# Kernel optimization log

Hardware: AMD Instinct MI355X
Metric: run time of the kernel (lower is better)

The kernel has to match this reference:

```python
import jax, jax.numpy as jnp
import numpy as np

B = 8192   # particle ensemble (vmapped y0)
T = 64     # timesteps
D = 2      # data_size
W = 128    # width_size
CAP = 5.0  # cap() clamps trajectories to a bounded domain


def setup_inputs() -> dict:
    key = jax.random.key(0)
    ks = jax.random.split(key, 10)
    s_in = 1.0 / np.sqrt(D)
    s_h = 1.0 / np.sqrt(W)
    u = jax.random.uniform
    return {
        "ts": jnp.linspace(0.0, 1.0, T, dtype=jnp.float32),
        "y0": jax.random.normal(ks[0], (B, D), jnp.float32),
        "W1": u(ks[1], (W, D), jnp.float32, -s_in, s_in),
        "b1": u(ks[2], (W,), jnp.float32, -s_in, s_in),
        "W2": u(ks[3], (W, W), jnp.float32, -s_h, s_h),
        "b2": u(ks[4], (W,), jnp.float32, -s_h, s_h),
        "W3": u(ks[5], (W, W), jnp.float32, -s_h, s_h),
        "b3": u(ks[6], (W,), jnp.float32, -s_h, s_h),
        "W4": u(ks[7], (D, W), jnp.float32, -s_h, s_h),
        "b4": u(ks[8], (D,), jnp.float32, -s_h, s_h),
    }


def _func(y, W1, b1, W2, b2, W3, b3, W4, b4):
    # eqx.nn.MLP(data_size -> data_size, width_size, depth=3),
    # activation=leaky_relu, final_activation=identity. y: [B, D]
    h = jax.nn.leaky_relu(y @ W1.T + b1)
    h = jax.nn.leaky_relu(h @ W2.T + b2)
    h = jax.nn.leaky_relu(h @ W3.T + b3)
    return h @ W4.T + b4


def reference(ts, y0, W1, b1, W2, b2, W3, b3, W4, b4):
    # MultiTerm(drift, ODETerm(func)) with Euler on the uniform grid ts:
    #   y_{n+1} = y_n + dt_n * (drift(t_n, y_n) + func(t_n, y_n))
    # drift vector field: f(t, y) = -y
    dts = ts[1:] - ts[:-1]  # [T-1]

    def step(y, dt):
        dy = -y + _func(y, W1, b1, W2, b2, W3, b3, W4, b4)
        y_new = y + dt * dy
        return y_new, y_new

    _, ys_tail = jax.lax.scan(step, y0, dts)          # [T-1, B, D]
    ys = jnp.concatenate([y0[None], ys_tail], axis=0)  # [T, B, D] == solution.ys
    return jnp.clip(ys, -CAP, CAP)  # cap(solution.ys)
```

## Files before the change

kernel.cpp:

```cpp
#include <hip/hip_runtime.h>

#define NB 8192
#define NT 64
#define FCAP 5.0f

typedef unsigned int u32;
typedef float f32x4 __attribute__((ext_vector_type(4)));
typedef __bf16 bf16x8 __attribute__((ext_vector_type(8)));
typedef u32 u32x4 __attribute__((ext_vector_type(4)));
typedef u32 u32x2 __attribute__((ext_vector_type(2)));

static __device__ __forceinline__ u32 pk2(float lo, float hi) {
  u32 r;
  asm("v_cvt_pk_bf16_f32 %0, %1, %2" : "=v"(r) : "v"(lo), "v"(hi));
  return r;
}
static __device__ __forceinline__ float clipc(float a) { return fminf(fmaxf(a, -FCAP), FCAP); }

static __device__ __forceinline__ bf16x8 mkfrag(const float* __restrict__ p) {
  f32x4 a = *(const f32x4*)p, b = *(const f32x4*)(p + 4);
  u32x4 wv = {pk2(a[0], a[1]), pk2(a[2], a[3]), pk2(b[0], b[1]), pk2(b[2], b[3])};
  return __builtin_bit_cast(bf16x8, wv);
}

#define MFMA16(A, B, C) __builtin_amdgcn_mfma_f32_16x16x32_bf16(A, B, C, 0, 0, 0)

#define LRELU4(C)                                                  \
  _Pragma("unroll") for (int r_ = 0; r_ < 4; ++r_) {               \
    C[r_] = fmaxf(C[r_], 0.01f * C[r_]);                           \
  }

__global__ __launch_bounds__(256, 2) void ode_kernel(
    const float* __restrict__ ts, const float* __restrict__ y0,
    const float* __restrict__ W1, const float* __restrict__ b1,
    const float* __restrict__ W2, const float* __restrict__ b2,
    const float* __restrict__ W3, const float* __restrict__ b3,
    const float* __restrict__ W4, const float* __restrict__ b4,
    float* __restrict__ out) {
  const int tid = threadIdx.x;
  const int wv = __builtin_amdgcn_readfirstlane(tid >> 6);
  const int l = tid & 63;
  const int g = l >> 4;
  const int c = l & 15;
  const int gp0 = blockIdx.x * 16;

  __shared__ alignas(16) u32 bufA[16 * 68];
  __shared__ alignas(16) u32 bufB[16 * 68];
  __shared__ alignas(16) float fbuf[16 * 8];

  bf16x8 aW2[2][4], aW3[2][4];
#pragma unroll
  for (int mt = 0; mt < 2; ++mt) {
    const int R = 32 * wv + 16 * mt + c;
#pragma unroll
    for (int kt = 0; kt < 4; ++kt) {
      aW2[mt][kt] = mkfrag(W2 + R * 128 + 32 * kt + 8 * g);
      aW3[mt][kt] = mkfrag(W3 + R * 128 + 32 * kt + 8 * g);
    }
  }
  bf16x8 aW1[2];
#pragma unroll
  for (int mt = 0; mt < 2; ++mt) {
    const int R = 32 * wv + 16 * mt + c;
    u32x4 f = {0, 0, 0, 0};
    if (g == 0) {
      f[0] = pk2(W1[2 * R], W1[2 * R + 1]);
      f[1] = pk2(b1[R], 0.f);
    }
    aW1[mt] = __builtin_bit_cast(bf16x8, f);
  }
  bf16x8 aW4;
  {
    u32x4 f = {0, 0, 0, 0};
    if (c < 2) {
      const float* s = W4 + c * 128 + 32 * wv + 8 * g;
      f32x4 a = *(const f32x4*)s, b = *(const f32x4*)(s + 4);
      f = (u32x4){pk2(a[0], a[1]), pk2(a[2], a[3]), pk2(b[0], b[1]), pk2(b[2], b[3])};
    }
    aW4 = __builtin_bit_cast(bf16x8, f);
  }
  f32x4 cb2[2], cb3[2];
#pragma unroll
  for (int mt = 0; mt < 2; ++mt) {
#pragma unroll
    for (int r = 0; r < 4; ++r) {
      const int row = 32 * wv + 16 * mt + 4 * g + r;
      cb2[mt][r] = b2[row];
      cb3[mt][r] = b3[row];
    }
  }
  const float b40 = b4[0], b41 = b4[1];

  float y1 = y0[(gp0 + c) * 2];
  float y2 = y0[(gp0 + c) * 2 + 1];

  if (wv == 0 && g == 0) {
    float2 st = {clipc(y1), clipc(y2)};
    *(float2*)(out + (gp0 + c) * 2) = st;
  }

  const f32x4 zero4 = {0.f, 0.f, 0.f, 0.f};
  const int wbase = 68 * c + 16 * wv + 2 * g;
  const int rbase = 68 * c + 4 * g;

#pragma unroll 1
  for (int t = 0; t < NT - 1; ++t) {
    const float dt = ts[t + 1] - ts[t];

    u32x4 byw = {0, 0, 0, 0};
    if (g == 0) {
      byw[0] = pk2(y1, y2);
      byw[1] = 0x3f80u;
    }
    const bf16x8 By = __builtin_bit_cast(bf16x8, byw);
    f32x4 C0 = MFMA16(aW1[0], By, zero4);
    f32x4 C1 = MFMA16(aW1[1], By, zero4);
    LRELU4(C0);
    LRELU4(C1);
    *(__shared__ u32x2*)&bufA[wbase]     = (u32x2){pk2(C0[0], C0[1]), pk2(C0[2], C0[3])};
    *(__shared__ u32x2*)&bufA[wbase + 8] = (u32x2){pk2(C1[0], C1[1]), pk2(C1[2], C1[3])};
    __syncthreads();

    f32x4 D0 = cb2[0], D1 = cb2[1];
#pragma unroll
    for (int kt = 0; kt < 4; ++kt) {
      const bf16x8 q =
          __builtin_bit_cast(bf16x8, *(const __shared__ u32x4*)&bufA[rbase + 16 * kt]);
      D0 = MFMA16(aW2[0][kt], q, D0);
      D1 = MFMA16(aW2[1][kt], q, D1);
    }
    LRELU4(D0);
    LRELU4(D1);
    *(__shared__ u32x2*)&bufB[wbase]     = (u32x2){pk2(D0[0], D0[1]), pk2(D0[2], D0[3])};
    *(__shared__ u32x2*)&bufB[wbase + 8] = (u32x2){pk2(D1[0], D1[1]), pk2(D1[2], D1[3])};
    __syncthreads();

    f32x4 E0 = cb3[0], E1 = cb3[1];
#pragma unroll
    for (int kt = 0; kt < 4; ++kt) {
      const bf16x8 q =
          __builtin_bit_cast(bf16x8, *(const __shared__ u32x4*)&bufB[rbase + 16 * kt]);
      E0 = MFMA16(aW3[0][kt], q, E0);
      E1 = MFMA16(aW3[1][kt], q, E1);
    }
    LRELU4(E0);
    LRELU4(E1);
    *(__shared__ u32x2*)&bufA[wbase]     = (u32x2){pk2(E0[0], E0[1]), pk2(E0[2], E0[3])};
    *(__shared__ u32x2*)&bufA[wbase + 8] = (u32x2){pk2(E1[0], E1[1]), pk2(E1[2], E1[3])};

    const bf16x8 q3 =
        __builtin_bit_cast(bf16x8, *(const __shared__ u32x4*)&bufA[rbase + 16 * wv]);
    f32x4 C4 = MFMA16(aW4, q3, zero4);
    if (g == 0)
      *(__shared__ float2*)&fbuf[c * 8 + wv * 2] = (float2){C4[0], C4[1]};
    __syncthreads();

    const float4 pa = *(const __shared__ float4*)&fbuf[c * 8];
    const float4 pb = *(const __shared__ float4*)&fbuf[c * 8 + 4];
    const float f0 = b40 + pa.x + pa.z + pb.x + pb.z;
    const float f1v = b41 + pa.y + pa.w + pb.y + pb.w;
    y1 += dt * (f0 - y1);
    y2 += dt * (f1v - y2);

    if (wv == 0 && g == 0) {
      float2 st = {clipc(y1), clipc(y2)};
      *(float2*)(out + (t + 1) * (NB * 2) + (gp0 + c) * 2) = st;
    }
  }
}

extern "C" void kernel_launch(void* const* d_in, const int* in_sizes, int n_in,
                              void* d_out, int out_size, void* d_ws, size_t ws_size,
                              hipStream_t stream) {
  const float* ts = (const float*)d_in[0];
  const float* y0 = (const float*)d_in[1];
  const float* W1 = (const float*)d_in[2];
  const float* b1 = (const float*)d_in[3];
  const float* W2 = (const float*)d_in[4];
  const float* b2 = (const float*)d_in[5];
  const float* W3 = (const float*)d_in[6];
  const float* b3 = (const float*)d_in[7];
  const float* W4 = (const float*)d_in[8];
  const float* b4 = (const float*)d_in[9];

  ode_kernel<<<NB / 16, 256, 0, stream>>>(ts, y0, W1, b1, W2, b2, W3, b3, W4, b4,
                                          (float*)d_out);
}
```

Before: 64.62 us.

## Collapse each block to a single wave computing all hidden rows without barriers

Each block now runs one 64-lane wave instead of four. That wave holds all W1/W2/W3/W4 fragments in registers and computes all eight 16-row tiles of every layer, with biases staged in LDS. This removes the three __syncthreads per timestep and the cross-wave reduction of the final layer through shared memory. In exchange, the per-wave MFMA dependency chain grows about fourfold, register pressure rises sharply and may cause spills, and fewer SIMDs per CU are occupied.

New measurement: 145.0 us. 2.24x slower.

```diff
diff --git a/kernel.cpp b/kernel.cpp
--- a/kernel.cpp
+++ b/kernel.cpp
@@ -25,43 +25,44 @@
 
 #define MFMA16(A, B, C) __builtin_amdgcn_mfma_f32_16x16x32_bf16(A, B, C, 0, 0, 0)
 
-#define LRELU4(C)                                                  \
-  _Pragma("unroll") for (int r_ = 0; r_ < 4; ++r_) {               \
-    C[r_] = fmaxf(C[r_], 0.01f * C[r_]);                           \
-  }
+static __device__ __forceinline__ f32x4 lrelu4(f32x4 v) {
+  return __builtin_elementwise_max(v, v * 0.01f);
+}
 
-__global__ __launch_bounds__(256, 2) void ode_kernel(
+__global__ __launch_bounds__(64, 1) void ode_kernel(
     const float* __restrict__ ts, const float* __restrict__ y0,
     const float* __restrict__ W1, const float* __restrict__ b1,
     const float* __restrict__ W2, const float* __restrict__ b2,
     const float* __restrict__ W3, const float* __restrict__ b3,
     const float* __restrict__ W4, const float* __restrict__ b4,
     float* __restrict__ out) {
-  const int tid = threadIdx.x;
-  const int wv = __builtin_amdgcn_readfirstlane(tid >> 6);
-  const int l = tid & 63;
+  const int l = threadIdx.x;
   const int g = l >> 4;
   const int c = l & 15;
   const int gp0 = blockIdx.x * 16;
 
-  __shared__ alignas(16) u32 bufA[16 * 68];
-  __shared__ alignas(16) u32 bufB[16 * 68];
-  __shared__ alignas(16) float fbuf[16 * 8];
+  __shared__ alignas(16) u32 buf[16 * 68];
+  __shared__ alignas(16) float bls[256];
 
-  bf16x8 aW2[2][4], aW3[2][4];
+  bls[l] = b2[l];
+  bls[64 + l] = b2[64 + l];
+  bls[128 + l] = b3[l];
+  bls[192 + l] = b3[64 + l];
+
+  bf16x8 aW2[8][4], aW3[8][4];
 #pragma unroll
-  for (int mt = 0; mt < 2; ++mt) {
-    const int R = 32 * wv + 16 * mt + c;
+  for (int mt = 0; mt < 8; ++mt) {
+    const int R = 16 * mt + c;
 #pragma unroll
     for (int kt = 0; kt < 4; ++kt) {
       aW2[mt][kt] = mkfrag(W2 + R * 128 + 32 * kt + 8 * g);
       aW3[mt][kt] = mkfrag(W3 + R * 128 + 32 * kt + 8 * g);
     }
   }
-  bf16x8 aW1[2];
+  bf16x8 aW1[8];
 #pragma unroll
-  for (int mt = 0; mt < 2; ++mt) {
-    const int R = 32 * wv + 16 * mt + c;
+  for (int mt = 0; mt < 8; ++mt) {
+    const int R = 16 * mt + c;
     u32x4 f = {0, 0, 0, 0};
     if (g == 0) {
       f[0] = pk2(W1[2 * R], W1[2 * R + 1]);
@@ -69,38 +70,30 @@
     }
     aW1[mt] = __builtin_bit_cast(bf16x8, f);
   }
-  bf16x8 aW4;
-  {
+  bf16x8 aW4[4];
+#pragma unroll
+  for (int kt = 0; kt < 4; ++kt) {
     u32x4 f = {0, 0, 0, 0};
     if (c < 2) {
-      const float* s = W4 + c * 128 + 32 * wv + 8 * g;
-      f32x4 a = *(const f32x4*)s, b = *(const f32x4*)(s + 4);
+      const float* p = W4 + c * 128 + 32 * kt + 8 * g;
+      f32x4 a = *(const f32x4*)p, b = *(const f32x4*)(p + 4);
       f = (u32x4){pk2(a[0], a[1]), pk2(a[2], a[3]), pk2(b[0], b[1]), pk2(b[2], b[3])};
     }
-    aW4 = __builtin_bit_cast(bf16x8, f);
-  }
-  f32x4 cb2[2], cb3[2];
-#pragma unroll
-  for (int mt = 0; mt < 2; ++mt) {
-#pragma unroll
-    for (int r = 0; r < 4; ++r) {
-      const int row = 32 * wv + 16 * mt + 4 * g + r;
-      cb2[mt][r] = b2[row];
-      cb3[mt][r] = b3[row];
-    }
+    aW4[kt] = __builtin_bit_cast(bf16x8, f);
   }
   const float b40 = b4[0], b41 = b4[1];
 
-  float y1 = y0[(gp0 + c) * 2];
-  float y2 = y0[(gp0 + c) * 2 + 1];
-
-  if (wv == 0 && g == 0) {
+  float y1 = 0.f, y2 = 0.f;
+  if (g == 0) {
+    const float2 yv = *(const float2*)(y0 + (gp0 + c) * 2);
+    y1 = yv.x;
+    y2 = yv.y;
     float2 st = {clipc(y1), clipc(y2)};
     *(float2*)(out + (gp0 + c) * 2) = st;
   }
 
   const f32x4 zero4 = {0.f, 0.f, 0.f, 0.f};
-  const int wbase = 68 * c + 16 * wv + 2 * g;
+  const int wbase = 68 * c + 2 * g;
   const int rbase = 68 * c + 4 * g;
 
 #pragma unroll 1
@@ -113,58 +106,74 @@
       byw[1] = 0x3f80u;
     }
     const bf16x8 By = __builtin_bit_cast(bf16x8, byw);
-    f32x4 C0 = MFMA16(aW1[0], By, zero4);
-    f32x4 C1 = MFMA16(aW1[1], By, zero4);
-    LRELU4(C0);
-    LRELU4(C1);
-    *(__shared__ u32x2*)&bufA[wbase]     = (u32x2){pk2(C0[0], C0[1]), pk2(C0[2], C0[3])};
-    *(__shared__ u32x2*)&bufA[wbase + 8] = (u32x2){pk2(C1[0], C1[1]), pk2(C1[2], C1[3])};
-    __syncthreads();
+    f32x4 C[8];
+#pragma unroll
+    for (int mt = 0; mt < 8; ++mt) C[mt] = MFMA16(aW1[mt], By, zero4);
+#pragma unroll
+    for (int mt = 0; mt < 8; ++mt) {
+      C[mt] = lrelu4(C[mt]);
+      *(__shared__ u32x2*)&buf[wbase + 8 * mt] =
+          (u32x2){pk2(C[mt][0], C[mt][1]), pk2(C[mt][2], C[mt][3])};
+    }
+    {
+      const bf16x8 q0 = __builtin_bit_cast(bf16x8, *(const __shared__ u32x4*)&buf[rbase]);
+      const bf16x8 q1 = __builtin_bit_cast(bf16x8, *(const __shared__ u32x4*)&buf[rbase + 16]);
+      const bf16x8 q2 = __builtin_bit_cast(bf16x8, *(const __shared__ u32x4*)&buf[rbase + 32]);
+      const bf16x8 q3 = __builtin_bit_cast(bf16x8, *(const __shared__ u32x4*)&buf[rbase + 48]);
+#pragma unroll
+      for (int mt = 0; mt < 8; ++mt) {
+        const f32x4 bias = *(const __shared__ f32x4*)&bls[16 * mt + 4 * g];
+        f32x4 a = MFMA16(aW2[mt][0], q0, bias);
+        a = MFMA16(aW2[mt][1], q1, a);
+        a = MFMA16(aW2[mt][2], q2, a);
+        C[mt] = MFMA16(aW2[mt][3], q3, a);
+      }
+    }
+#pragma unroll
+    for (int mt = 0; mt < 8; ++mt) {
+      C[mt] = lrelu4(C[mt]);
+      *(__shared__ u32x2*)&buf[wbase + 8 * mt] =
+          (u32x2){pk2(C[mt][0], C[mt][1]), pk2(C[mt][2], C[mt][3])};
+    }
+    {
+      const bf16x8 q0 = __builtin_bit_cast(bf16x8, *(const __shared__ u32x4*)&buf[rbase]);
+      const bf16x8 q1 = __builtin_bit_cast(bf16x8, *(const __shared__ u32x4*)&buf[rbase + 16]);
+      const bf16x8 q2 = __builtin_bit_cast(bf16x8, *(const __shared__ u32x4*)&buf[rbase + 32]);
+      const bf16x8 q3 = __builtin_bit_cast(bf16x8, *(const __shared__ u32x4*)&buf[rbase + 48]);
+#pragma unroll
+      for (int mt = 0; mt < 8; ++mt) {
+        const f32x4 bias = *(const __shared__ f32x4*)&bls[128 + 16 * mt + 4 * g];
+        f32x4 a = MFMA16(aW3[mt][0], q0, bias);
+        a = MFMA16(aW3[mt][1], q1, a);
+        a = MFMA16(aW3[mt][2], q2, a);
+        C[mt] = MFMA16(aW3[mt][3], q3, a);
+      }
+    }
+#pragma unroll
+    for (int mt = 0; mt < 8; ++mt) {
+      C[mt] = lrelu4(C[mt]);
+      *(__shared__ u32x2*)&buf[wbase + 8 * mt] =
+          (u32x2){pk2(C[mt][0], C[mt][1]), pk2(C[mt][2], C[mt][3])};
+    }
+    {
+      const bf16x8 q0 = __builtin_bit_cast(bf16x8, *(const __shared__ u32x4*)&buf[rbase]);
+      const bf16x8 q1 = __builtin_bit_cast(bf16x8, *(const __shared__ u32x4*)&buf[rbase + 16]);
+      const bf16x8 q2 = __builtin_bit_cast(bf16x8, *(const __shared__ u32x4*)&buf[rbase + 32]);
+      const bf16x8 q3 = __builtin_bit_cast(bf16x8, *(const __shared__ u32x4*)&buf[rbase + 48]);
+      f32x4 D = MFMA16(aW4[0], q0, zero4);
+      f32x4 E = MFMA16(aW4[1], q1, zero4);
+      D = MFMA16(aW4[2], q2, D);
+      E = MFMA16(aW4[3], q3, E);
+      const f32x4 C4 = D + E;
 
-    f32x4 D0 = cb2[0], D1 = cb2[1];
-#pragma unroll
-    for (int kt = 0; kt < 4; ++kt) {
-      const bf16x8 q =
-          __builtin_bit_cast(bf16x8, *(const __shared__ u32x4*)&bufA[rbase + 16 * kt]);
-      D0 = MFMA16(aW2[0][kt], q, D0);
-      D1 = MFMA16(aW2[1][kt], q, D1);
-    }
-    LRELU4(D0);
-    LRELU4(D1);
-    *(__shared__ u32x2*)&bufB[wbase]     = (u32x2){pk2(D0[0], D0[1]), pk2(D0[2], D0[3])};
-    *(__shared__ u32x2*)&bufB[wbase + 8] = (u32x2){pk2(D1[0], D1[1]), pk2(D1[2], D1[3])};
-    __syncthreads();
-
-    f32x4 E0 = cb3[0], E1 = cb3[1];
-#pragma unroll
-    for (int kt = 0; kt < 4; ++kt) {
-      const bf16x8 q =
-          __builtin_bit_cast(bf16x8, *(const __shared__ u32x4*)&bufB[rbase + 16 * kt]);
-      E0 = MFMA16(aW3[0][kt], q, E0);
-      E1 = MFMA16(aW3[1][kt], q, E1);
-    }
-    LRELU4(E0);
-    LRELU4(E1);
-    *(__shared__ u32x2*)&bufA[wbase]     = (u32x2){pk2(E0[0], E0[1]), pk2(E0[2], E0[3])};
-    *(__shared__ u32x2*)&bufA[wbase + 8] = (u32x2){pk2(E1[0], E1[1]), pk2(E1[2], E1[3])};
-
-    const bf16x8 q3 =
-        __builtin_bit_cast(bf16x8, *(const __shared__ u32x4*)&bufA[rbase + 16 * wv]);
-    f32x4 C4 = MFMA16(aW4, q3, zero4);
-    if (g == 0)
-      *(__shared__ float2*)&fbuf[c * 8 + wv * 2] = (float2){C4[0], C4[1]};
-    __syncthreads();
-
-    const float4 pa = *(const __shared__ float4*)&fbuf[c * 8];
-    const float4 pb = *(const __shared__ float4*)&fbuf[c * 8 + 4];
-    const float f0 = b40 + pa.x + pa.z + pb.x + pb.z;
-    const float f1v = b41 + pa.y + pa.w + pb.y + pb.w;
-    y1 += dt * (f0 - y1);
-    y2 += dt * (f1v - y2);
-
-    if (wv == 0 && g == 0) {
-      float2 st = {clipc(y1), clipc(y2)};
-      *(float2*)(out + (t + 1) * (NB * 2) + (gp0 + c) * 2) = st;
+      if (g == 0) {
+        const float f0 = C4[0] + b40;
+        const float f1v = C4[1] + b41;
+        y1 += dt * (f0 - y1);
+        y2 += dt * (f1v - y2);
+        float2 st = {clipc(y1), clipc(y2)};
+        *(float2*)(out + (t + 1) * (NB * 2) + (gp0 + c) * 2) = st;
+      }
     }
   }
 }
@@ -183,6 +192,6 @@
   const float* W4 = (const float*)d_in[8];
   const float* b4 = (const float*)d_in[9];
 
-  ode_kernel<<<NB / 16, 256, 0, stream>>>(ts, y0, W1, b1, W2, b2, W3, b3, W4, b4,
-                                          (float*)d_out);
+  ode_kernel<<<NB / 16, 64, 0, stream>>>(ts, y0, W1, b1, W2, b2, W3, b3, W4, b4,
+                                         (float*)d_out);
 }
```

## Interleave two particle groups per block to overlap MLP layer dependency chains

Applied to the files above, without the earlier changes.

Each block now handles 32 particles as two independent groups of 16, with the layer stages of the two groups staggered so one group's MFMA chain fills the other's barrier and dependency stalls. The final layer is computed redundantly in every wave over all K tiles, which removes the cross-wave partial-sum reduction buffer. The K-loop is also split into two accumulator chains to shorten MFMA dependency latency. The trade-offs are half as many blocks (256), a launch bound that now targets one block per CU, more LDS, and duplicated layer-4 work.

Result: slower. 108.2 us (+67.5%).

```diff
diff --git a/kernel.cpp b/kernel.cpp
--- a/kernel.cpp
+++ b/kernel.cpp
@@ -25,12 +25,11 @@
 
 #define MFMA16(A, B, C) __builtin_amdgcn_mfma_f32_16x16x32_bf16(A, B, C, 0, 0, 0)
 
-#define LRELU4(C)                                                  \
-  _Pragma("unroll") for (int r_ = 0; r_ < 4; ++r_) {               \
-    C[r_] = fmaxf(C[r_], 0.01f * C[r_]);                           \
-  }
-
-__global__ __launch_bounds__(256, 2) void ode_kernel(
+static __device__ __forceinline__ f32x4 lrelu4(f32x4 v) {
+  return __builtin_elementwise_max(v, v * 0.01f);
+}
+
+__global__ __launch_bounds__(256, 1) void ode_kernel(
     const float* __restrict__ ts, const float* __restrict__ y0,
     const float* __restrict__ W1, const float* __restrict__ b1,
     const float* __restrict__ W2, const float* __restrict__ b2,
@@ -42,11 +41,10 @@
   const int l = tid & 63;
   const int g = l >> 4;
   const int c = l & 15;
-  const int gp0 = blockIdx.x * 16;
-
-  __shared__ alignas(16) u32 bufA[16 * 68];
-  __shared__ alignas(16) u32 bufB[16 * 68];
-  __shared__ alignas(16) float fbuf[16 * 8];
+  const int gp0 = blockIdx.x * 32;
+
+  __shared__ alignas(16) u32 hx1[16 * 68], hx2[16 * 68], hx3[16 * 68];
+  __shared__ alignas(16) u32 hy1[16 * 68], hy2[16 * 68], hy3[16 * 68];
 
   bf16x8 aW2[2][4], aW3[2][4];
 #pragma unroll
@@ -69,15 +67,16 @@
     }
     aW1[mt] = __builtin_bit_cast(bf16x8, f);
   }
-  bf16x8 aW4;
-  {
+  bf16x8 aW4[4];
+#pragma unroll
+  for (int kt = 0; kt < 4; ++kt) {
     u32x4 f = {0, 0, 0, 0};
     if (c < 2) {
-      const float* s = W4 + c * 128 + 32 * wv + 8 * g;
-      f32x4 a = *(const f32x4*)s, b = *(const f32x4*)(s + 4);
+      const float* p = W4 + c * 128 + 32 * kt + 8 * g;
+      f32x4 a = *(const f32x4*)p, b = *(const f32x4*)(p + 4);
       f = (u32x4){pk2(a[0], a[1]), pk2(a[2], a[3]), pk2(b[0], b[1]), pk2(b[2], b[3])};
     }
-    aW4 = __builtin_bit_cast(bf16x8, f);
+    aW4[kt] = __builtin_bit_cast(bf16x8, f);
   }
   f32x4 cb2[2], cb3[2];
 #pragma unroll
@@ -91,81 +90,98 @@
   }
   const float b40 = b4[0], b41 = b4[1];
 
-  float y1 = y0[(gp0 + c) * 2];
-  float y2 = y0[(gp0 + c) * 2 + 1];
-
-  if (wv == 0 && g == 0) {
-    float2 st = {clipc(y1), clipc(y2)};
-    *(float2*)(out + (gp0 + c) * 2) = st;
+  float yx1 = 0.f, yx2 = 0.f, yy1 = 0.f, yy2 = 0.f;
+  if (g == 0) {
+    const float2 a = *(const float2*)(y0 + (gp0 + c) * 2);
+    const float2 b = *(const float2*)(y0 + (gp0 + 16 + c) * 2);
+    yx1 = a.x; yx2 = a.y;
+    yy1 = b.x; yy2 = b.y;
+    if (wv == 0) {
+      *(float2*)(out + (gp0 + c) * 2)      = (float2){clipc(yx1), clipc(yx2)};
+      *(float2*)(out + (gp0 + 16 + c) * 2) = (float2){clipc(yy1), clipc(yy2)};
+    }
   }
 
   const f32x4 zero4 = {0.f, 0.f, 0.f, 0.f};
   const int wbase = 68 * c + 16 * wv + 2 * g;
   const int rbase = 68 * c + 4 * g;
 
-#pragma unroll 1
-  for (int t = 0; t < NT - 1; ++t) {
-    const float dt = ts[t + 1] - ts[t];
-
+  auto L1 = [&](u32* dst, float y1, float y2) {
     u32x4 byw = {0, 0, 0, 0};
     if (g == 0) {
       byw[0] = pk2(y1, y2);
       byw[1] = 0x3f80u;
     }
     const bf16x8 By = __builtin_bit_cast(bf16x8, byw);
-    f32x4 C0 = MFMA16(aW1[0], By, zero4);
-    f32x4 C1 = MFMA16(aW1[1], By, zero4);
-    LRELU4(C0);
-    LRELU4(C1);
-    *(__shared__ u32x2*)&bufA[wbase]     = (u32x2){pk2(C0[0], C0[1]), pk2(C0[2], C0[3])};
-    *(__shared__ u32x2*)&bufA[wbase + 8] = (u32x2){pk2(C1[0], C1[1]), pk2(C1[2], C1[3])};
-    __syncthreads();
-
-    f32x4 D0 = cb2[0], D1 = cb2[1];
-#pragma unroll
-    for (int kt = 0; kt < 4; ++kt) {
-      const bf16x8 q =
-          __builtin_bit_cast(bf16x8, *(const __shared__ u32x4*)&bufA[rbase + 16 * kt]);
-      D0 = MFMA16(aW2[0][kt], q, D0);
-      D1 = MFMA16(aW2[1][kt], q, D1);
-    }
-    LRELU4(D0);
-    LRELU4(D1);
-    *(__shared__ u32x2*)&bufB[wbase]     = (u32x2){pk2(D0[0], D0[1]), pk2(D0[2], D0[3])};
-    *(__shared__ u32x2*)&bufB[wbase + 8] = (u32x2){pk2(D1[0], D1[1]), pk2(D1[2], D1[3])};
-    __syncthreads();
-
-    f32x4 E0 = cb3[0], E1 = cb3[1];
-#pragma unroll
-    for (int kt = 0; kt < 4; ++kt) {
-      const bf16x8 q =
-          __builtin_bit_cast(bf16x8, *(const __shared__ u32x4*)&bufB[rbase + 16 * kt]);
-      E0 = MFMA16(aW3[0][kt], q, E0);
-      E1 = MFMA16(aW3[1][kt], q, E1);
-    }
-    LRELU4(E0);
-    LRELU4(E1);
-    *(__shared__ u32x2*)&bufA[wbase]     = (u32x2){pk2(E0[0], E0[1]), pk2(E0[2], E0[3])};
-    *(__shared__ u32x2*)&bufA[wbase + 8] = (u32x2){pk2(E1[0], E1[1]), pk2(E1[2], E1[3])};
-
-    const bf16x8 q3 =
-        __builtin_bit_cast(bf16x8, *(const __shared__ u32x4*)&bufA[rbase + 16 * wv]);
-    f32x4 C4 = MFMA16(aW4, q3, zero4);
-    if (g == 0)
-      *(__shared__ float2*)&fbuf[c * 8 + wv * 2] = (float2){C4[0], C4[1]};
-    __syncthreads();
-
-    const float4 pa = *(const __shared__ float4*)&fbuf[c * 8];
-    const float4 pb = *(const __shared__ float4*)&fbuf[c * 8 + 4];
-    const float f0 = b40 + pa.x + pa.z + pb.x + pb.z;
-    const float f1v = b41 + pa.y + pa.w + pb.y + pb.w;
-    y1 += dt * (f0 - y1);
-    y2 += dt * (f1v - y2);
-
-    if (wv == 0 && g == 0) {
-      float2 st = {clipc(y1), clipc(y2)};
-      *(float2*)(out + (t + 1) * (NB * 2) + (gp0 + c) * 2) = st;
-    }
+    const f32x4 C0 = lrelu4(MFMA16(aW1[0], By, zero4));
+    const f32x4 C1 = lrelu4(MFMA16(aW1[1], By, zero4));
+    *(__shared__ u32x2*)&dst[wbase]     = (u32x2){pk2(C0[0], C0[1]), pk2(C0[2], C0[3])};
+    *(__shared__ u32x2*)&dst[wbase + 8] = (u32x2){pk2(C1[0], C1[1]), pk2(C1[2], C1[3])};
+  };
+  auto L23 = [&](const u32* src, u32* dst, const bf16x8 (&A)[2][4], const f32x4 (&cb)[2]) {
+    const bf16x8 q0 = __builtin_bit_cast(bf16x8, *(const __shared__ u32x4*)&src[rbase]);
+    const bf16x8 q1 = __builtin_bit_cast(bf16x8, *(const __shared__ u32x4*)&src[rbase + 16]);
+    const bf16x8 q2 = __builtin_bit_cast(bf16x8, *(const __shared__ u32x4*)&src[rbase + 32]);
+    const bf16x8 q3 = __builtin_bit_cast(bf16x8, *(const __shared__ u32x4*)&src[rbase + 48]);
+    f32x4 D0 = MFMA16(A[0][0], q0, cb[0]);
+    f32x4 D1 = MFMA16(A[1][0], q0, cb[1]);
+    f32x4 E0 = MFMA16(A[0][1], q1, zero4);
+    f32x4 E1 = MFMA16(A[1][1], q1, zero4);
+    D0 = MFMA16(A[0][2], q2, D0);
+    D1 = MFMA16(A[1][2], q2, D1);
+    E0 = MFMA16(A[0][3], q3, E0);
+    E1 = MFMA16(A[1][3], q3, E1);
+    const f32x4 C0 = lrelu4(D0 + E0);
+    const f32x4 C1 = lrelu4(D1 + E1);
+    *(__shared__ u32x2*)&dst[wbase]     = (u32x2){pk2(C0[0], C0[1]), pk2(C0[2], C0[3])};
+    *(__shared__ u32x2*)&dst[wbase + 8] = (u32x2){pk2(C1[0], C1[1]), pk2(C1[2], C1[3])};
+  };
+  auto L4E = [&](const u32* src, float& y1, float& y2, float dt, int t, int pofs) {
+    const bf16x8 q0 = __builtin_bit_cast(bf16x8, *(const __shared__ u32x4*)&src[rbase]);
+    const bf16x8 q1 = __builtin_bit_cast(bf16x8, *(const __shared__ u32x4*)&src[rbase + 16]);
+    const bf16x8 q2 = __builtin_bit_cast(bf16x8, *(const __shared__ u32x4*)&src[rbase + 32]);
+    const bf16x8 q3 = __builtin_bit_cast(bf16x8, *(const __shared__ u32x4*)&src[rbase + 48]);
+    f32x4 D = MFMA16(aW4[0], q0, zero4);
+    f32x4 E = MFMA16(aW4[1], q1, zero4);
+    D = MFMA16(aW4[2], q2, D);
+    E = MFMA16(aW4[3], q3, E);
+    const f32x4 C4 = D + E;
+    if (g == 0) {
+      const float f0 = C4[0] + b40;
+      const float f1v = C4[1] + b41;
+      y1 += dt * (f0 - y1);
+      y2 += dt * (f1v - y2);
+      if (wv == 0) {
+        *(float2*)(out + (t + 1) * (NB * 2) + (gp0 + pofs + c) * 2) =
+            (float2){clipc(y1), clipc(y2)};
+      }
+    }
+  };
+
+  L1(hx1, yx1, yx2);
+  __syncthreads();
+  L23(hx1, hx2, aW2, cb2);
+  __syncthreads();
+
+#pragma unroll 1
+  for (int t = 0; t < NT - 1; ++t) {
+    const float dt = ts[t + 1] - ts[t];
+
+    L23(hx2, hx3, aW3, cb3);
+    L1(hy1, yy1, yy2);
+    __syncthreads();
+
+    L4E(hx3, yx1, yx2, dt, t, 0);
+    L23(hy1, hy2, aW2, cb2);
+    __syncthreads();
+
+    if (t < NT - 2) L1(hx1, yx1, yx2);
+    L23(hy2, hy3, aW3, cb3);
+    __syncthreads();
+
+    if (t < NT - 2) L23(hx1, hx2, aW2, cb2);
+    L4E(hy3, yy1, yy2, dt, t, 16);
+    __syncthreads();
   }
 }
 
@@ -183,6 +199,6 @@
   const float* W4 = (const float*)d_in[8];
   const float* b4 = (const float*)d_in[9];
 
-  ode_kernel<<<NB / 16, 256, 0, stream>>>(ts, y0, W1, b1, W2, b2, W3, b3, W4, b4,
+  ode_kernel<<<NB / 32, 256, 0, stream>>>(ts, y0, W1, b1, W2, b2, W3, b3, W4, b4,
                                           (float*)d_out);
 }
```
